# Optimization experiments

Measured on AMD Instinct MI355X. Metric: run time of the kernel, lower is better.

The kernel has to match this reference:

```python
import jax, jax.numpy as jnp
import numpy as np

TEMPERATURE = 1.0
EPS = 1e-5
COS_EPS = 1e-8  # torch CosineSimilarity default eps
N_POS, N_NEG, D = 512, 512, 512


def setup_inputs() -> dict:
    key = jax.random.key(0)
    k1, k2, k3 = jax.random.split(key, 3)
    tensor_positive = jax.random.normal(k1, (N_POS, D), dtype=jnp.float32)
    tensor_negative = jax.random.normal(k2, (N_NEG, D), dtype=jnp.float32)
    # nn.Linear(512*3, 1), weight ~ N(0, 0.02^2), bias zeros
    linear_w = jax.random.normal(k3, (1, 3 * D), dtype=jnp.float32) * 0.02
    linear_b = jnp.zeros((1,), dtype=jnp.float32)
    return {"tensor_positive": tensor_positive, "tensor_negative": tensor_negative,
            "linear_w": linear_w, "linear_b": linear_b}


def _cos_matrix(a, b):
    # pairwise cosine similarity [Na, Nb], matching torch CosineSimilarity eps clamp
    an = a / jnp.maximum(jnp.linalg.norm(a, axis=-1, keepdims=True), COS_EPS)
    bn = b / jnp.maximum(jnp.linalg.norm(b, axis=-1, keepdims=True), COS_EPS)
    return an @ bn.T


def reference(tensor_positive, tensor_negative, linear_w, linear_b):
    pos, neg = tensor_positive, tensor_negative
    n_pos, d = pos.shape
    n_neg = neg.shape[0]

    # NCE part
    logit_n = jnp.exp(_cos_matrix(pos, neg) / TEMPERATURE)        # [N, M]
    deno_n = jnp.sum(logit_n, axis=-1)                            # [N]
    logit_p = jnp.exp(_cos_matrix(pos, pos) / TEMPERATURE)        # [N, N]
    loss = jnp.sum(-jnp.log(logit_p / (deno_n[:, None] + logit_p + EPS)))

    # Pairwise classifier: linear(cat([a, b, |a-b|])) decomposed as
    # a@w1 + b@w2 + |a-b|@w3 to avoid materializing the 3D concat.
    w = linear_w[0]
    w1, w2, w3 = w[:d], w[d:2 * d], w[2 * d:]
    allv = jnp.concatenate([pos, neg], axis=0)                    # [N+M, D]
    t1 = pos @ w1                                                 # [N]
    t2 = allv @ w2                                                # [N+M]
    diff = jnp.abs(pos[:, None, :] - allv[None, :, :])            # [N, N+M, D]
    t3 = jnp.einsum('nmd,d->nm', diff, w3)                        # [N, N+M]
    logits = t1[:, None] + t2[None, :] + t3 + linear_b[0]
    labels = jnp.concatenate([jnp.ones((n_pos,), jnp.float32),
                              jnp.zeros((n_neg,), jnp.float32)])  # [N+M]
    # BCE(sigmoid(logits), labels), stable form; per-i mean then sum over i
    bce = labels[None, :] * jax.nn.softplus(-logits) + (1.0 - labels[None, :]) * jax.nn.softplus(logits)
    loss = loss + jnp.sum(jnp.mean(bce, axis=1))
    return loss
```

## Files before the change

kernel.cpp:

```cpp
#include <hip/hip_runtime.h>
#include <math.h>

#define NPOS 512
#define DIM  512
#define NB   1024
#define EPSV 1e-5f
#define COS_EPS 1e-8f

#define OFF_INV 0
#define OFF_T1  1024
#define OFF_T2  1536
#define OFF_P   2560
#define PSZ     (NPOS * NB)

__device__ __forceinline__ float softplus_f(float x) {
    return fmaxf(x, 0.f) + __logf(1.f + __expf(-fabsf(x)));
}

__global__ __launch_bounds__(256) void prep_kernel(
    const float* __restrict__ pos, const float* __restrict__ neg,
    const float* __restrict__ w, float* __restrict__ ws, float* __restrict__ out)
{
    int gtid = blockIdx.x * 256 + threadIdx.x;
    if (gtid == 0) out[0] = 0.f;
    int row  = gtid >> 6;
    int lane = threadIdx.x & 63;
    if (row >= NB) return;
    bool is_pos = row < NPOS;
    const float* r = is_pos ? pos + row * DIM : neg + (row - NPOS) * DIM;

    const float4* r4  = (const float4*)r + lane * 2;
    const float4* w14 = (const float4*)(w) + lane * 2;
    const float4* w24 = (const float4*)(w + DIM) + lane * 2;
    float4 a0 = r4[0],  a1 = r4[1];
    float4 u0 = w14[0], u1 = w14[1];
    float4 v0 = w24[0], v1 = w24[1];

    float ss  = a0.x*a0.x + a0.y*a0.y + a0.z*a0.z + a0.w*a0.w
              + a1.x*a1.x + a1.y*a1.y + a1.z*a1.z + a1.w*a1.w;
    float dw1 = a0.x*u0.x + a0.y*u0.y + a0.z*u0.z + a0.w*u0.w
              + a1.x*u1.x + a1.y*u1.y + a1.z*u1.z + a1.w*u1.w;
    float dw2 = a0.x*v0.x + a0.y*v0.y + a0.z*v0.z + a0.w*v0.w
              + a1.x*v1.x + a1.y*v1.y + a1.z*v1.z + a1.w*v1.w;

    #pragma unroll
    for (int off = 32; off; off >>= 1) {
        ss  += __shfl_xor(ss, off);
        dw1 += __shfl_xor(dw1, off);
        dw2 += __shfl_xor(dw2, off);
    }
    if (lane == 0) {
        float inv = 1.f / fmaxf(sqrtf(ss), COS_EPS);
        ws[OFF_INV + row] = inv;
        ws[OFF_T2 + row]  = dw2;
        if (is_pos) ws[OFF_T1 + row] = dw1;
    }
}

__global__ __launch_bounds__(256, 1) void fused_kernel(
    const float* __restrict__ pos, const float* __restrict__ neg,
    const float* __restrict__ w, float* __restrict__ ws)
{
    __shared__ __align__(16) float As[128][68];
    __shared__ __align__(16) float Bs[128][68];

    const int tid = threadIdx.x;
    const int m0 = blockIdx.x * 128;
    const int n0 = blockIdx.y * 128;
    const int z  = blockIdx.z;

    const float* Asrc = pos + (size_t)n0 * DIM + z * 64;
    const float* Bsrc = ((m0 < NPOS) ? (pos + (size_t)m0 * DIM)
                                     : (neg + (size_t)(m0 - NPOS) * DIM)) + z * 64;
    const float* w3 = w + 2 * DIM + z * 64;

    const int lr = tid >> 4;
    const int lc = (tid & 15) << 2;
    #pragma unroll
    for (int q = 0; q < 8; ++q) {
        int row = lr + 16 * q;
        *(float4*)&As[row][lc] = *(const float4*)(Asrc + (size_t)row * DIM + lc);
        *(float4*)&Bs[row][lc] = *(const float4*)(Bsrc + (size_t)row * DIM + lc);
    }
    __syncthreads();

    const int ti = tid >> 4;
    const int tj = tid & 15;

    float c[8][8] = {{0.f}};
    float t[8][8] = {{0.f}};

    #pragma unroll 2
    for (int k = 0; k < 64; k += 4) {
        const float4 wv = *(const float4*)(w3 + k);
        float4 bv[8];
        #pragma unroll
        for (int s = 0; s < 8; ++s) bv[s] = *(const float4*)&Bs[tj + 16 * s][k];
        #pragma unroll
        for (int r = 0; r < 8; ++r) {
            const float4 av = *(const float4*)&As[ti + 16 * r][k];
            #pragma unroll
            for (int s = 0; s < 8; ++s) {
                c[r][s] = fmaf(av.x, bv[s].x, c[r][s]);
                c[r][s] = fmaf(av.y, bv[s].y, c[r][s]);
                c[r][s] = fmaf(av.z, bv[s].z, c[r][s]);
                c[r][s] = fmaf(av.w, bv[s].w, c[r][s]);
                t[r][s] = fmaf(fabsf(av.x - bv[s].x), wv.x, t[r][s]);
                t[r][s] = fmaf(fabsf(av.y - bv[s].y), wv.y, t[r][s]);
                t[r][s] = fmaf(fabsf(av.z - bv[s].z), wv.z, t[r][s]);
                t[r][s] = fmaf(fabsf(av.w - bv[s].w), wv.w, t[r][s]);
            }
        }
    }

    float* Sp = ws + OFF_P + (size_t)z * PSZ;
    float* Tp = ws + OFF_P + (size_t)(8 + z) * PSZ;
    #pragma unroll
    for (int r = 0; r < 8; ++r) {
        int n = n0 + ti + 16 * r;
        #pragma unroll
        for (int s = 0; s < 8; ++s) {
            int m = m0 + tj + 16 * s;
            Sp[(size_t)n * NB + m] = c[r][s];
            Tp[(size_t)n * NB + m] = t[r][s];
        }
    }
}

__global__ __launch_bounds__(256) void finish_kernel(
    const float* __restrict__ lb, const float* __restrict__ ws, float* __restrict__ out)
{
    __shared__ float eneg_s[4];
    __shared__ float red[4];

    const int n  = blockIdx.x;
    const int wv = threadIdx.x >> 6;
    const int l  = threadIdx.x & 63;
    const int i4 = wv * 64 + l;

    float4 sc = {0.f, 0.f, 0.f, 0.f};
    float4 tt = {0.f, 0.f, 0.f, 0.f};
    #pragma unroll
    for (int z = 0; z < 8; ++z) {
        const float4 s = ((const float4*)(ws + OFF_P + (size_t)z * PSZ + (size_t)n * NB))[i4];
        const float4 p = ((const float4*)(ws + OFF_P + (size_t)(8 + z) * PSZ + (size_t)n * NB))[i4];
        sc.x += s.x; sc.y += s.y; sc.z += s.z; sc.w += s.w;
        tt.x += p.x; tt.y += p.y; tt.z += p.z; tt.w += p.w;
    }

    const float invn = ws[OFF_INV + n];
    const float4 inv4 = *(const float4*)(ws + OFF_INV + 4 * i4);
    float4 cc;
    cc.x = sc.x * invn * inv4.x;
    cc.y = sc.y * invn * inv4.y;
    cc.z = sc.z * invn * inv4.z;
    cc.w = sc.w * invn * inv4.w;

    float ep = 0.f;
    if (wv >= 2)
        ep = __expf(cc.x) + __expf(cc.y) + __expf(cc.z) + __expf(cc.w);
    #pragma unroll
    for (int off = 32; off; off >>= 1) ep += __shfl_xor(ep, off);
    if (l == 0) eneg_s[wv] = ep;
    __syncthreads();
    const float eneg = eneg_s[2] + eneg_s[3];

    float part = 0.f;
    if (wv < 2) {
        part += __logf(eneg + __expf(cc.x) + EPSV) - cc.x;
        part += __logf(eneg + __expf(cc.y) + EPSV) - cc.y;
        part += __logf(eneg + __expf(cc.z) + EPSV) - cc.z;
        part += __logf(eneg + __expf(cc.w) + EPSV) - cc.w;
    }

    const float t1n  = ws[OFF_T1 + n];
    const float bias = lb[0];
    const float4 t2 = *(const float4*)(ws + OFF_T2 + 4 * i4);
    float lgx = t1n + t2.x + tt.x + bias;
    float lgy = t1n + t2.y + tt.y + bias;
    float lgz = t1n + t2.z + tt.z + bias;
    float lgw = t1n + t2.w + tt.w + bias;
    float b;
    if (wv < 2)
        b = softplus_f(-lgx) + softplus_f(-lgy) + softplus_f(-lgz) + softplus_f(-lgw);
    else
        b = softplus_f(lgx) + softplus_f(lgy) + softplus_f(lgz) + softplus_f(lgw);
    part += b * (1.f / 1024.f);

    #pragma unroll
    for (int off = 32; off; off >>= 1) part += __shfl_xor(part, off);
    if (l == 0) red[wv] = part;
    __syncthreads();
    if (threadIdx.x == 0)
        atomicAdd(out, red[0] + red[1] + red[2] + red[3]);
}

extern "C" void kernel_launch(void* const* d_in, const int* in_sizes, int n_in,
                              void* d_out, int out_size, void* d_ws, size_t ws_size,
                              hipStream_t stream) {
    (void)in_sizes; (void)n_in; (void)out_size; (void)ws_size;
    const float* pos = (const float*)d_in[0];
    const float* neg = (const float*)d_in[1];
    const float* w   = (const float*)d_in[2];
    const float* lb  = (const float*)d_in[3];
    float* out = (float*)d_out;
    float* ws  = (float*)d_ws;

    prep_kernel<<<256, 256, 0, stream>>>(pos, neg, w, ws, out);
    fused_kernel<<<dim3(8, 4, 8), 256, 0, stream>>>(pos, neg, w, ws);
    finish_kernel<<<512, 256, 0, stream>>>(lb, ws, out);
}
```

Before: 120.9 us.

## Split cosine matmul onto bf16 MFMA kernel and retile L1-distance kernel

The cosine-similarity dot products move out of the fused FP32 kernel into a separate kernel that uses bf16 MFMA instructions on bf16 copies of the inputs written by the prep kernel. That kernel applies the normalisation directly, so only one S matrix is written instead of eight K-split partials. The remaining |a-b|·w3 kernel uses smaller 64x128 tiles with transposed, swizzled shared-memory layouts and two blocks per CU for more occupancy. The cost is reduced precision in the cosine term from the bf16 rounding, plus one extra kernel launch.

```diff
diff --git a/kernel.cpp b/kernel.cpp
--- a/kernel.cpp
+++ b/kernel.cpp
@@ -10,11 +10,24 @@
 #define OFF_INV 0
 #define OFF_T1  1024
 #define OFF_T2  1536
-#define OFF_P   2560
+#define OFF_S   2560
 #define PSZ     (NPOS * NB)
+#define OFF_TP  (OFF_S + PSZ)
+#define OFF_BF  (OFF_TP + 8 * PSZ)
+
+#define FSW(x) ((x) + 4 * ((x) >> 5))
+
+typedef __attribute__((ext_vector_type(8))) __bf16 bf16x8;
+typedef __attribute__((ext_vector_type(4))) float  f32x4;
 
 __device__ __forceinline__ float softplus_f(float x) {
     return fmaxf(x, 0.f) + __logf(1.f + __expf(-fabsf(x)));
+}
+
+__device__ __forceinline__ unsigned short f2bf(float f) {
+    union { float f; unsigned int u; } v; v.f = f;
+    unsigned int r = (v.u + 0x7fffu + ((v.u >> 16) & 1u)) >> 16;
+    return (unsigned short)r;
 }
 
 __global__ __launch_bounds__(256) void prep_kernel(
@@ -36,6 +49,13 @@
     float4 u0 = w14[0], u1 = w14[1];
     float4 v0 = w24[0], v1 = w24[1];
 
+    uint4 pk;
+    pk.x = (unsigned)f2bf(a0.x) | ((unsigned)f2bf(a0.y) << 16);
+    pk.y = (unsigned)f2bf(a0.z) | ((unsigned)f2bf(a0.w) << 16);
+    pk.z = (unsigned)f2bf(a1.x) | ((unsigned)f2bf(a1.y) << 16);
+    pk.w = (unsigned)f2bf(a1.z) | ((unsigned)f2bf(a1.w) << 16);
+    ((uint4*)(ws + OFF_BF))[row * 64 + lane] = pk;
+
     float ss  = a0.x*a0.x + a0.y*a0.y + a0.z*a0.z + a0.w*a0.w
               + a1.x*a1.x + a1.y*a1.y + a1.z*a1.z + a1.w*a1.w;
     float dw1 = a0.x*u0.x + a0.y*u0.y + a0.z*u0.z + a0.w*u0.w
@@ -57,73 +77,105 @@
     }
 }
 
-__global__ __launch_bounds__(256, 1) void fused_kernel(
+__global__ __launch_bounds__(256) void cosmat_mfma(
+    float* __restrict__ ws)
+{
+    const int wave = (blockIdx.x * 256 + threadIdx.x) >> 6;
+    const int lane = threadIdx.x & 63;
+    const int n0 = (wave >> 6) << 4;
+    const int m0 = (wave & 63) << 4;
+    const int rc   = lane & 15;
+    const int quad = lane >> 4;
+
+    const unsigned short* bf = (const unsigned short*)(ws + OFF_BF);
+    const bf16x8* pa = (const bf16x8*)(bf + (n0 + rc) * DIM + quad * 8);
+    const bf16x8* pb = (const bf16x8*)(bf + (m0 + rc) * DIM + quad * 8);
+
+    f32x4 acc = {0.f, 0.f, 0.f, 0.f};
+    #pragma unroll
+    for (int k = 0; k < 16; ++k)
+        acc = __builtin_amdgcn_mfma_f32_16x16x32_bf16(pa[4 * k], pb[4 * k], acc, 0, 0, 0);
+
+    float* S = ws + OFF_S;
+    const float invm = ws[OFF_INV + m0 + rc];
+    #pragma unroll
+    for (int e = 0; e < 4; ++e) {
+        int n = n0 + quad * 4 + e;
+        S[(size_t)n * NB + m0 + rc] = acc[e] * ws[OFF_INV + n] * invm;
+    }
+}
+
+__global__ __launch_bounds__(256, 2) void t3_kernel(
     const float* __restrict__ pos, const float* __restrict__ neg,
     const float* __restrict__ w, float* __restrict__ ws)
 {
-    __shared__ __align__(16) float As[128][68];
-    __shared__ __align__(16) float Bs[128][68];
+    __shared__ __align__(16) float As[64][68];
+    __shared__ __align__(16) float Bs[64][140];
 
     const int tid = threadIdx.x;
     const int m0 = blockIdx.x * 128;
-    const int n0 = blockIdx.y * 128;
-    const int z  = blockIdx.z;
-
-    const float* Asrc = pos + (size_t)n0 * DIM + z * 64;
+    const int n0 = blockIdx.y * 64;
+    const int kb = blockIdx.z * 64;
+
+    const float* Asrc = pos + (size_t)n0 * DIM + kb;
     const float* Bsrc = ((m0 < NPOS) ? (pos + (size_t)m0 * DIM)
-                                     : (neg + (size_t)(m0 - NPOS) * DIM)) + z * 64;
-    const float* w3 = w + 2 * DIM + z * 64;
-
-    const int lr = tid >> 4;
-    const int lc = (tid & 15) << 2;
-    #pragma unroll
-    for (int q = 0; q < 8; ++q) {
-        int row = lr + 16 * q;
-        *(float4*)&As[row][lc] = *(const float4*)(Asrc + (size_t)row * DIM + lc);
-        *(float4*)&Bs[row][lc] = *(const float4*)(Bsrc + (size_t)row * DIM + lc);
+                                     : (neg + (size_t)(m0 - NPOS) * DIM)) + kb;
+    const float* w3 = w + 2 * DIM + kb;
+
+    {
+        const int r = tid >> 2, g = (tid & 3) * 16;
+        #pragma unroll
+        for (int u = 0; u < 4; ++u) {
+            float4 v = *(const float4*)(Asrc + (size_t)r * DIM + g + 4 * u);
+            As[g + 4 * u + 0][r] = v.x;
+            As[g + 4 * u + 1][r] = v.y;
+            As[g + 4 * u + 2][r] = v.z;
+            As[g + 4 * u + 3][r] = v.w;
+        }
+    }
+    {
+        const int r = tid >> 1, h = (tid & 1) * 32;
+        const int fr = FSW(r);
+        #pragma unroll
+        for (int u = 0; u < 8; ++u) {
+            float4 v = *(const float4*)(Bsrc + (size_t)r * DIM + h + 4 * u);
+            Bs[h + 4 * u + 0][fr] = v.x;
+            Bs[h + 4 * u + 1][fr] = v.y;
+            Bs[h + 4 * u + 2][fr] = v.z;
+            Bs[h + 4 * u + 3][fr] = v.w;
+        }
     }
     __syncthreads();
 
-    const int ti = tid >> 4;
-    const int tj = tid & 15;
-
-    float c[8][8] = {{0.f}};
-    float t[8][8] = {{0.f}};
-
-    #pragma unroll 2
-    for (int k = 0; k < 64; k += 4) {
-        const float4 wv = *(const float4*)(w3 + k);
-        float4 bv[8];
+    const int n4 = (tid & 15) * 4;
+    const int m8 = (tid >> 4) * 8;
+    const int fm = FSW(m8);
+
+    float acc[4][8] = {{0.f}};
+
+    #pragma unroll 4
+    for (int k = 0; k < 64; ++k) {
+        const float4 av = *(const float4*)&As[k][n4];
+        const float4 b0 = *(const float4*)&Bs[k][fm];
+        const float4 b1 = *(const float4*)&Bs[k][fm + 4];
+        const float wk = w3[k];
+        const float a[4] = {av.x, av.y, av.z, av.w};
+        const float b[8] = {b0.x, b0.y, b0.z, b0.w, b1.x, b1.y, b1.z, b1.w};
         #pragma unroll
-        for (int s = 0; s < 8; ++s) bv[s] = *(const float4*)&Bs[tj + 16 * s][k];
-        #pragma unroll
-        for (int r = 0; r < 8; ++r) {
-            const float4 av = *(const float4*)&As[ti + 16 * r][k];
+        for (int r = 0; r < 4; ++r)
             #pragma unroll
-            for (int s = 0; s < 8; ++s) {
-                c[r][s] = fmaf(av.x, bv[s].x, c[r][s]);
-                c[r][s] = fmaf(av.y, bv[s].y, c[r][s]);
-                c[r][s] = fmaf(av.z, bv[s].z, c[r][s]);
-                c[r][s] = fmaf(av.w, bv[s].w, c[r][s]);
-                t[r][s] = fmaf(fabsf(av.x - bv[s].x), wv.x, t[r][s]);
-                t[r][s] = fmaf(fabsf(av.y - bv[s].y), wv.y, t[r][s]);
-                t[r][s] = fmaf(fabsf(av.z - bv[s].z), wv.z, t[r][s]);
-                t[r][s] = fmaf(fabsf(av.w - bv[s].w), wv.w, t[r][s]);
-            }
-        }
-    }
-
-    float* Sp = ws + OFF_P + (size_t)z * PSZ;
-    float* Tp = ws + OFF_P + (size_t)(8 + z) * PSZ;
-    #pragma unroll
-    for (int r = 0; r < 8; ++r) {
-        int n = n0 + ti + 16 * r;
-        #pragma unroll
-        for (int s = 0; s < 8; ++s) {
-            int m = m0 + tj + 16 * s;
-            Sp[(size_t)n * NB + m] = c[r][s];
-            Tp[(size_t)n * NB + m] = t[r][s];
-        }
+            for (int s = 0; s < 8; ++s)
+                acc[r][s] = fmaf(fabsf(a[r] - b[s]), wk, acc[r][s]);
+    }
+
+    float* Tp = ws + OFF_TP + (size_t)blockIdx.z * PSZ;
+    #pragma unroll
+    for (int r = 0; r < 4; ++r) {
+        int n = n0 + n4 + r;
+        float4 o0 = {acc[r][0], acc[r][1], acc[r][2], acc[r][3]};
+        float4 o1 = {acc[r][4], acc[r][5], acc[r][6], acc[r][7]};
+        *(float4*)(Tp + (size_t)n * NB + m0 + m8)     = o0;
+        *(float4*)(Tp + (size_t)n * NB + m0 + m8 + 4) = o1;
     }
 }
 
@@ -138,23 +190,14 @@
     const int l  = threadIdx.x & 63;
     const int i4 = wv * 64 + l;
 
-    float4 sc = {0.f, 0.f, 0.f, 0.f};
+    const float4 cc = ((const float4*)(ws + OFF_S + (size_t)n * NB))[i4];
+
     float4 tt = {0.f, 0.f, 0.f, 0.f};
     #pragma unroll
     for (int z = 0; z < 8; ++z) {
-        const float4 s = ((const float4*)(ws + OFF_P + (size_t)z * PSZ + (size_t)n * NB))[i4];
-        const float4 p = ((const float4*)(ws + OFF_P + (size_t)(8 + z) * PSZ + (size_t)n * NB))[i4];
-        sc.x += s.x; sc.y += s.y; sc.z += s.z; sc.w += s.w;
+        const float4 p = ((const float4*)(ws + OFF_TP + (size_t)z * PSZ + (size_t)n * NB))[i4];
         tt.x += p.x; tt.y += p.y; tt.z += p.z; tt.w += p.w;
     }
-
-    const float invn = ws[OFF_INV + n];
-    const float4 inv4 = *(const float4*)(ws + OFF_INV + 4 * i4);
-    float4 cc;
-    cc.x = sc.x * invn * inv4.x;
-    cc.y = sc.y * invn * inv4.y;
-    cc.z = sc.z * invn * inv4.z;
-    cc.w = sc.w * invn * inv4.w;
 
     float ep = 0.f;
     if (wv >= 2)
@@ -207,6 +250,7 @@
     float* ws  = (float*)d_ws;
 
     prep_kernel<<<256, 256, 0, stream>>>(pos, neg, w, ws, out);
-    fused_kernel<<<dim3(8, 4, 8), 256, 0, stream>>>(pos, neg, w, ws);
+    cosmat_mfma<<<512, 256, 0, stream>>>(ws);
+    t3_kernel<<<dim3(8, 8, 8), 256, 0, stream>>>(pos, neg, w, ws);
     finish_kernel<<<512, 256, 0, stream>>>(lb, ws, out);
 }
```

Measured after the change: 110.7 us. 1.09x faster.
